# Kernel tuning notes

Hardware: AMD Instinct MI355X
Metric: run time of the kernel (lower is better)

## Reference

```python
import jax, jax.numpy as jnp
import numpy as np
import math

EMBED_DIM = 1024
NUM_HEADS = 16
HEAD_DIM = EMBED_DIM // NUM_HEADS
BLOCK_SIZE = 64
NUM_RAND_BLOCKS = 3
B, L = 2, 2048


def _build_sparse_mask(seq_len, block_size, num_rand_blocks, seed=0):
    """BigBird block-sparse mask: global (first/last block) + window (prev/self/next) + random blocks."""
    nb = seq_len // block_size
    bm = np.zeros((nb, nb), dtype=bool)
    # global: first and last blocks attend to all / are attended by all
    bm[0, :] = True
    bm[:, 0] = True
    bm[-1, :] = True
    bm[:, -1] = True
    # sliding window for interior blocks
    for b in range(1, nb - 1):
        bm[b, max(b - 1, 0):b + 2] = True
    # random blocks for interior blocks (deterministic for reproducibility)
    rng = np.random.default_rng(seed)
    for b in range(1, nb - 1):
        avail = [x for x in range(nb) if x != b]
        picks = rng.permutation(len(avail))[:num_rand_blocks]
        for p in picks:
            bm[b, avail[p]] = True
    # expand block mask to token-level [L, L]
    return np.kron(bm, np.ones((block_size, block_size), dtype=bool))


def setup_inputs() -> dict:
    key = jax.random.key(0)
    k0, k1, k2, k3, k4 = jax.random.split(key, 5)
    hidden_states = jax.random.normal(k0, (B, L, EMBED_DIM), dtype=jnp.float32)
    s = 0.02
    # torch nn.Linear weights have shape [out_features, in_features]
    Wq = jax.random.normal(k1, (EMBED_DIM, EMBED_DIM), dtype=jnp.float32) * s
    Wk = jax.random.normal(k2, (EMBED_DIM, EMBED_DIM), dtype=jnp.float32) * s
    Wv = jax.random.normal(k3, (EMBED_DIM, EMBED_DIM), dtype=jnp.float32) * s
    Wo = jax.random.normal(k4, (EMBED_DIM, EMBED_DIM), dtype=jnp.float32) * s
    sparse_mask = jnp.asarray(_build_sparse_mask(L, BLOCK_SIZE, NUM_RAND_BLOCKS))
    return {"hidden_states": hidden_states, "Wq": Wq, "Wk": Wk, "Wv": Wv,
            "Wo": Wo, "sparse_mask": sparse_mask}


def reference(hidden_states, Wq, Wk, Wv, Wo, sparse_mask):
    Bsz, Lq, D = hidden_states.shape
    H, hd = NUM_HEADS, HEAD_DIM
    # projections (Linear no bias): x @ W.T
    q = (hidden_states @ Wq.T).reshape(Bsz, Lq, H, hd).transpose(0, 2, 1, 3)
    k = (hidden_states @ Wk.T).reshape(Bsz, Lq, H, hd).transpose(0, 2, 1, 3)
    v = (hidden_states @ Wv.T).reshape(Bsz, Lq, H, hd).transpose(0, 2, 1, 3)
    # dense scores with block-sparse mask (matches reference module's math)
    scores = jnp.einsum('bhqd,bhkd->bhqk', q, k) / math.sqrt(hd)  # [B,H,L,L]
    scores = jnp.where(sparse_mask[None, None, :, :], scores, -jnp.inf)
    attn = jax.nn.softmax(scores.astype(jnp.float32), axis=-1).astype(scores.dtype)
    out = jnp.einsum('bhqk,bhkd->bhqd', attn, v)
    out = out.transpose(0, 2, 1, 3).reshape(Bsz, Lq, D)
    out = out @ Wo.T
    return out
```

## Files before the change

kernel.cpp:

```cpp
#include <hip/hip_runtime.h>
#include <hip/hip_bf16.h>
#include <stdint.h>

#define LSEQ   2048
#define DMODEL 1024
#define NHEADS 16
#define HDIM   64
#define NB     32
#define BATCH  2
#define NGRP   38
#define NWG_ATTN (32 * NGRP)

typedef unsigned short u16;
typedef __attribute__((ext_vector_type(8))) __bf16 bf16x8;
typedef __attribute__((ext_vector_type(4))) float f32x4;
typedef __attribute__((ext_vector_type(4))) unsigned int u32x4;
typedef __attribute__((ext_vector_type(4))) u16 u16x4;


__device__ __forceinline__ u16 f2b(float f) {
  unsigned b = __float_as_uint(f);
  return (u16)((b + 0x7FFFu + ((b >> 16) & 1u)) >> 16);
}

__device__ __forceinline__ void lds_dma16(const u16* g, u16* l) {
  __builtin_amdgcn_global_load_lds(
      (__attribute__((address_space(1))) const void*)g,
      (__attribute__((address_space(3))) void*)l, 16, 0, 0);
}

__device__ __forceinline__ bool probe_is_bf16(const void* src) {
  const u16* p = (const u16*)src;
  int cnt = 0;
  #pragma unroll
  for (int i = 0; i < 64; ++i) {
    int e = (p[i] >> 7) & 0xFF;
    cnt += (e >= 100 && e <= 140) ? 1 : 0;
  }
  return cnt >= 48;
}

__device__ __forceinline__ bool mask_block(const void* m, int qb, int kb) {
  const unsigned char* p = (const unsigned char*)m;
  size_t e = (size_t)(qb * 64) * LSEQ + (size_t)kb * 64;
  unsigned char b0 = p[0], b1 = p[1], b2 = p[2];
  if (b0 == 1 && b1 == 1) return p[e] != 0;
  if (b0 == 1 && b1 == 0 && b2 == 1) return ((const u16*)m)[e] != 0;
  if (b0 == 1) return ((const unsigned int*)m)[e] != 0;
  if (b0 == 0x80 && b1 == 0x3f) return ((const u16*)m)[e] != 0;
  return ((const float*)m)[e] != 0.0f;
}

__global__ __launch_bounds__(256) void convert_kernel(
    const void* __restrict__ hs, const void* __restrict__ wq,
    const void* __restrict__ wk, const void* __restrict__ wv,
    const void* __restrict__ wo, u16* __restrict__ dst,
    const void* __restrict__ mask, int* __restrict__ skb,
    f32x4* __restrict__ zbuf, int zn4) {
  __shared__ int sflags;
  if (threadIdx.x == 0)
    sflags = (probe_is_bf16(hs) ? 1 : 0) | (probe_is_bf16(wq) ? 2 : 0);
  __syncthreads();
  bool bf_hs = (sflags & 1) != 0, bf_w = (sflags & 2) != 0;
  if (blockIdx.x == 0 && threadIdx.x < NB) {
    int qb = threadIdx.x;
    int base = (qb == 0) ? 0 : ((qb == 31) ? 32 : (64 + (qb - 1) * 8));
    int cap = (qb == 0 || qb == 31) ? 32 : 8;
    int c = 0;
    for (int kb = 0; kb < NB; ++kb)
      if (mask_block(mask, qb, kb)) skb[base + c++] = kb;
    for (; c < cap; ++c) skb[base + c] = -1;
  }
  const int HS4 = BATCH * LSEQ * DMODEL / 4;
  const int W4 = DMODEL * DMODEL / 4;
  int total4 = HS4 + 4 * W4;
  int stride = gridDim.x * blockDim.x;
  if (!(bf_hs && bf_w)) {
    for (int i = blockIdx.x * blockDim.x + threadIdx.x; i < total4; i += stride) {
      const void* src;
      int off;
      bool isbf;
      if (i < HS4) { src = hs; off = i; isbf = bf_hs; }
      else {
        int j = i - HS4;
        int wsel = j >> 18;
        off = j & (W4 - 1);
        src = (wsel == 0) ? wq : (wsel == 1) ? wk : (wsel == 2) ? wv : wo;
        isbf = bf_w;
      }
      if (isbf) continue;
      f32x4 f = ((const f32x4*)src)[off];
      ((u16x4*)dst)[i] = (u16x4){f2b(f[0]), f2b(f[1]), f2b(f[2]), f2b(f[3])};
    }
  }
  for (int i = blockIdx.x * blockDim.x + threadIdx.x; i < zn4; i += stride)
    zbuf[i] = (f32x4){0.f, 0.f, 0.f, 0.f};
}

#define QBM 256
#define QBN 192

#define BAR()  __builtin_amdgcn_s_barrier()
#define LGK0() asm volatile("s_waitcnt lgkmcnt(0)" ::: "memory")
#define VM3()  asm volatile("s_waitcnt vmcnt(3)" ::: "memory")
#define VM0()  asm volatile("s_waitcnt vmcnt(0)" ::: "memory")

#define STG_A1(p, gi, kt) \
    lds_dma16(Abase + (gi)*65536 + (kt)*64, sA + (p)*16384 + (gi)*4096 + wb8)
#define STG_B1(p, Bgp, kt) \
    lds_dma16((Bgp) + (kt)*64, sB + (p)*12288 + (Bgp##_gi)*4096 + wb8)

#define LDA(afX, p, mh) do { \
    const u16* _ba = sA + (p)*16384 + (wr*128 + (mh)*64 + lc)*64; \
    afX[0][0] = *(const bf16x8*)(_ba +        x0); afX[0][1] = *(const bf16x8*)(_ba +        x1); \
    afX[1][0] = *(const bf16x8*)(_ba + 1024 + x0); afX[1][1] = *(const bf16x8*)(_ba + 1024 + x1); \
    afX[2][0] = *(const bf16x8*)(_ba + 2048 + x0); afX[2][1] = *(const bf16x8*)(_ba + 2048 + x1); \
    afX[3][0] = *(const bf16x8*)(_ba + 3072 + x0); afX[3][1] = *(const bf16x8*)(_ba + 3072 + x1); \
  } while (0)
#define LDB1(p, nh) do { \
    const u16* _bb = sB + (p)*12288 + (wc*48 + (nh)*16 + lc)*64; \
    bfr[nh][0] = *(const bf16x8*)(_bb + x0); bfr[nh][1] = *(const bf16x8*)(_bb + x1); \
  } while (0)

#define MM8(afX, mh, nh) do { \
    __builtin_amdgcn_s_setprio(1); \
    _Pragma("unroll") \
    for (int _m = 0; _m < 4; ++_m) { \
      f32x4 _c = acc[(mh)*4+_m][nh]; \
      _c = __builtin_amdgcn_mfma_f32_16x16x32_bf16(afX[_m][0], bfr[nh][0], _c, 0, 0, 0); \
      _c = __builtin_amdgcn_mfma_f32_16x16x32_bf16(afX[_m][1], bfr[nh][1], _c, 0, 0, 0); \
      acc[(mh)*4+_m][nh] = _c; \
    } \
    __builtin_amdgcn_s_setprio(0); \
  } while (0)

__global__ __launch_bounds__(512, 2) void gemm_qkv(
    const void* __restrict__ hs_raw, const u16* __restrict__ hs_cv,
    const void* __restrict__ wq_r, const void* __restrict__ wk_r,
    const void* __restrict__ wv_r, const u16* __restrict__ wqb_cv,
    u16* __restrict__ C, u16* __restrict__ C2) {
  extern __shared__ u16 smem[];
  u16* sA = smem;
  u16* sB = smem + 2 * 16384;

  const int t = threadIdx.x;
  const int l = t & 63;
  const int w = t >> 6;
  const int wr = w >> 2;
  const int wc = w & 3;
  const int q4 = l >> 4, lc = l & 15;
  const int tileM = blockIdx.x * QBM;
  const int tileN = blockIdx.y * QBN;
  const int sr = t >> 3;
  const int scs = (((t & 7) ^ ((t >> 3) & 7)) * 8);
  const int wb8 = w * 512;
  const int x0 = (q4 ^ (lc & 7)) * 8;
  const int x1 = x0 ^ 32;

  const bool a_bf = probe_is_bf16(hs_raw);
  const bool b_bf = probe_is_bf16(wq_r);
  const u16* Asrc = a_bf ? (const u16*)hs_raw : hs_cv;
  const u16* Abase = Asrc + (size_t)(tileM + sr) * 1024 + scs;
  const u16* Bg0; const u16* Bg1; const u16* Bg2;
  {
    int g0 = tileN, g1 = tileN + 64, g2 = tileN + 128;
    const void* w0 = (g0 >> 10) == 0 ? wq_r : (g0 >> 10) == 1 ? wk_r : wv_r;
    const void* w1 = (g1 >> 10) == 0 ? wq_r : (g1 >> 10) == 1 ? wk_r : wv_r;
    const void* w2 = (g2 >> 10) == 0 ? wq_r : (g2 >> 10) == 1 ? wk_r : wv_r;
    Bg0 = (b_bf ? (const u16*)w0 + (size_t)(g0 & 1023) * 1024
                : wqb_cv + (size_t)g0 * 1024) + (size_t)sr * 1024 + scs;
    Bg1 = (b_bf ? (const u16*)w1 + (size_t)(g1 & 1023) * 1024
                : wqb_cv + (size_t)g1 * 1024) + (size_t)sr * 1024 + scs;
    Bg2 = (b_bf ? (const u16*)w2 + (size_t)(g2 & 1023) * 1024
                : wqb_cv + (size_t)g2 * 1024) + (size_t)sr * 1024 + scs;
  }
  const int Bg0_gi = 0, Bg1_gi = 1, Bg2_gi = 2;

  f32x4 acc[8][3] = {};
  bf16x8 afA[4][2];
  bf16x8 afB[4][2];
  bf16x8 bfr[3][2];

  STG_B1(0, Bg0, 0); STG_B1(0, Bg1, 0); STG_B1(0, Bg2, 0);
  STG_A1(0, 0, 0); STG_A1(0, 1, 0); STG_A1(0, 2, 0); STG_A1(0, 3, 0);
  STG_B1(1, Bg0, 1); STG_B1(1, Bg1, 1); STG_B1(1, Bg2, 1);
  VM3(); BAR();

  #pragma unroll 1
  for (int j = 0; j < 7; ++j) {
    const int kt1 = 2 * j + 1, ktn0 = 2 * j + 2, ktn1 = 2 * j + 3;
    LDA(afA, 0, 0); LDB1(0, 0); LDB1(0, 1); STG_A1(1, 0, kt1); STG_A1(1, 1, kt1);
    BAR(); LGK0(); MM8(afA, 0, 0); MM8(afA, 0, 1); BAR();
    LDB1(0, 2); LDA(afB, 0, 1); STG_A1(1, 2, kt1); STG_A1(1, 3, kt1);
    BAR(); LGK0(); MM8(afA, 0, 2); MM8(afB, 1, 0); BAR();
    STG_B1(0, Bg0, ktn0); STG_B1(0, Bg1, ktn0); STG_B1(0, Bg2, ktn0);
    VM3(); BAR(); MM8(afB, 1, 1); MM8(afB, 1, 2); BAR();
    LDA(afA, 1, 0); LDB1(1, 0); LDB1(1, 1); STG_A1(0, 0, ktn0); STG_A1(0, 1, ktn0);
    BAR(); LGK0(); MM8(afA, 0, 0); MM8(afA, 0, 1); BAR();
    LDB1(1, 2); LDA(afB, 1, 1); STG_A1(0, 2, ktn0); STG_A1(0, 3, ktn0);
    BAR(); LGK0(); MM8(afA, 0, 2); MM8(afB, 1, 0); BAR();
    STG_B1(1, Bg0, ktn1); STG_B1(1, Bg1, ktn1); STG_B1(1, Bg2, ktn1);
    VM3(); BAR(); MM8(afB, 1, 1); MM8(afB, 1, 2); BAR();
  }

  LDA(afA, 0, 0); LDB1(0, 0); LDB1(0, 1); STG_A1(1, 0, 15); STG_A1(1, 1, 15);
  BAR(); LGK0(); MM8(afA, 0, 0); MM8(afA, 0, 1); BAR();
  LDB1(0, 2); LDA(afB, 0, 1); STG_A1(1, 2, 15); STG_A1(1, 3, 15);
  BAR(); LGK0(); MM8(afA, 0, 2); MM8(afB, 1, 0); BAR();
  VM0(); BAR(); MM8(afB, 1, 1); MM8(afB, 1, 2); BAR();
  LDA(afA, 1, 0); LDB1(1, 0); LDB1(1, 1);
  LGK0(); MM8(afA, 0, 0); MM8(afA, 0, 1);
  LDB1(1, 2); LDA(afB, 1, 1);
  LGK0(); MM8(afA, 0, 2); MM8(afB, 1, 0);
  MM8(afB, 1, 1); MM8(afB, 1, 2);

  #pragma unroll
  for (int im = 0; im < 8; ++im)
    #pragma unroll
    for (int jn = 0; jn < 3; ++jn) {
      int rowb = tileM + wr * 128 + im * 16 + q4 * 4;
      int col = tileN + wc * 48 + jn * 16 + lc;
      int sel = col >> 10;
      int o = col & 1023;
      int h = o >> 6, d = o & 63;
      int b = rowb >> 11, ll = rowb & 2047;
      if (sel == 2) {
        u16x4 pk = {f2b(acc[im][jn][0]), f2b(acc[im][jn][1]),
                    f2b(acc[im][jn][2]), f2b(acc[im][jn][3])};
        *(u16x4*)(C2 + ((size_t)((b * NHEADS + h) * HDIM + d)) * LSEQ + ll) = pk;
      } else {
        float scl = (sel == 0) ? 0.125f : 1.0f;
        #pragma unroll
        for (int r = 0; r < 4; ++r) {
          size_t idx = (size_t)sel * (size_t)(BATCH * NHEADS * LSEQ * HDIM) +
                       (((size_t)(b * NHEADS + h) * LSEQ) + ll + r) * HDIM + d;
          C[idx] = f2b(acc[im][jn][r] * scl);
        }
      }
    }
}

#define OTK 32

__global__ __launch_bounds__(256) void gemm_out(
    const u16* __restrict__ A, const void* __restrict__ wo_raw,
    const u16* __restrict__ wo_cv, void* __restrict__ C,
    const void* __restrict__ probe_src) {
  __shared__ u16 lA[128 * OTK];
  __shared__ u16 lB[64 * OTK];
  int t = threadIdx.x;
  int w = t >> 6, l = t & 63, q4 = l >> 4, lc = l & 15;
  int lr = l >> 2, lcc = l & 3;
  int tileM = blockIdx.x * 128, tileN = blockIdx.y * 64;
  int wm = (w >> 1) * 64, wn = (w & 1) * 32;
  bool out_bf = probe_is_bf16(probe_src);
  const u16* Bsrc = probe_is_bf16(wo_raw) ? (const u16*)wo_raw : wo_cv;

  f32x4 acc[4][2] = {};

  for (int kt = 0; kt < 1024; kt += OTK) {
    __syncthreads();
    #pragma unroll
    for (int it = 0; it < 2; ++it) {
      int m = w * 2 + it;
      int row = m * 16 + lr;
      lds_dma16(A + (size_t)(tileM + row) * 1024 + kt + lcc * 8, lA + m * 512);
    }
    {
      int row = w * 16 + lr;
      lds_dma16(Bsrc + (size_t)(tileN + row) * 1024 + kt + lcc * 8, lB + w * 512);
    }
    __syncthreads();
    bf16x8 af[4], bf[2];
    #pragma unroll
    for (int i = 0; i < 4; ++i)
      af[i] = *(const bf16x8*)(lA + (wm + i * 16 + lc) * OTK + q4 * 8);
    #pragma unroll
    for (int j = 0; j < 2; ++j)
      bf[j] = *(const bf16x8*)(lB + (wn + j * 16 + lc) * OTK + q4 * 8);
    #pragma unroll
    for (int i = 0; i < 4; ++i)
      #pragma unroll
      for (int j = 0; j < 2; ++j)
        acc[i][j] = __builtin_amdgcn_mfma_f32_16x16x32_bf16(af[i], bf[j], acc[i][j], 0, 0, 0);
  }

  #pragma unroll
  for (int i = 0; i < 4; ++i)
    #pragma unroll
    for (int j = 0; j < 2; ++j) {
      int rowb = tileM + wm + i * 16 + q4 * 4;
      int col = tileN + wn + j * 16 + lc;
      #pragma unroll
      for (int r = 0; r < 4; ++r) {
        float v = acc[i][j][r];
        size_t idx = (size_t)(rowb + r) * 1024 + col;
        if (out_bf) ((u16*)C)[idx] = f2b(v);
        else ((float*)C)[idx] = v;
      }
    }
}

#define LDP 72

__global__ __launch_bounds__(256) void attn_kernel(
    const u16* __restrict__ qb_, const u16* __restrict__ kb_,
    const u16* __restrict__ vt_, const int* __restrict__ skb,
    float* __restrict__ obuf2, float* __restrict__ lbuf2,
    u16* __restrict__ ctx) {
  __shared__ u16 lK[2][64 * 64];
  __shared__ u16 lV[2][64 * 64];
  __shared__ u16 lP[4][16 * LDP];
  int i = blockIdx.x;
  int bh = (i & 7) + ((i >> 3) & 3) * 8;
  int g = i >> 5;
  int qb = (g < 4) ? 0 : ((g < 8) ? 31 : (g - 7));
  int t = threadIdx.x, w = t >> 6, l = t & 63, q4 = l >> 4, lc = l & 15;
  int r0 = t >> 3, r1 = 32 + (t >> 3);
  int scc = ((t & 7) ^ ((t >> 3) & 7)) * 8;
  const int x0 = (q4 ^ (lc & 7)) * 8;
  const int x1 = x0 ^ 32;

  const u16* qp = qb_ + ((size_t)bh * LSEQ + qb * 64 + w * 16 + lc) * HDIM;
  bf16x8 bq0 = *(const bf16x8*)(qp + q4 * 8);
  bf16x8 bq1 = *(const bf16x8*)(qp + 32 + q4 * 8);

  const u16* kp = kb_ + (size_t)bh * LSEQ * HDIM;
  const u16* vp = vt_ + (size_t)bh * HDIM * LSEQ;
  u16* myP = &lP[w][0];

  f32x4 oacc[4];
  #pragma unroll
  for (int d = 0; d < 4; ++d) oacc[d] = (f32x4){0.f, 0.f, 0.f, 0.f};
  float lp = 0.0f;

  int nkb = 0;
  #pragma unroll
  for (int j = 0; j < 8; ++j) nkb += (skb[g * 8 + j] >= 0) ? 1 : 0;

  auto STAGE = [&](int it, int buf) {
    int kb = skb[g * 8 + it];
    const u16* kblk = kp + (size_t)kb * 64 * HDIM;
    const u16* vblk = vp + kb * 64;
    u16* dK = &lK[buf][0];
    u16* dV = &lV[buf][0];
    lds_dma16(kblk + r0 * HDIM + scc, dK + w * 512);
    lds_dma16(kblk + r1 * HDIM + scc, dK + 2048 + w * 512);
    lds_dma16(vblk + (size_t)r0 * LSEQ + scc, dV + w * 512);
    lds_dma16(vblk + (size_t)r1 * LSEQ + scc, dV + 2048 + w * 512);
  };

  STAGE(0, 0);
  __syncthreads();

  for (int it = 0; it < nkb; ++it) {
    int buf = it & 1;
    if (it + 1 < nkb) STAGE(it + 1, buf ^ 1);
    const u16* bK = &lK[buf][0];
    const u16* bV = &lV[buf][0];

    f32x4 st[4];
    #pragma unroll
    for (int mt = 0; mt < 4; ++mt) {
      const u16* kr = bK + (mt * 16 + lc) * 64;
      bf16x8 k0 = *(const bf16x8*)(kr + x0);
      bf16x8 k1 = *(const bf16x8*)(kr + x1);
      f32x4 z = (f32x4){0.f, 0.f, 0.f, 0.f};
      z = __builtin_amdgcn_mfma_f32_16x16x32_bf16(k0, bq0, z, 0, 0, 0);
      z = __builtin_amdgcn_mfma_f32_16x16x32_bf16(k1, bq1, z, 0, 0, 0);
      st[mt] = z;
    }

    #pragma unroll
    for (int mt = 0; mt < 4; ++mt) {
      float p0 = __expf(st[mt][0]), p1 = __expf(st[mt][1]);
      float p2 = __expf(st[mt][2]), p3 = __expf(st[mt][3]);
      lp += (p0 + p1) + (p2 + p3);
      u16x4 pk = {f2b(p0), f2b(p1), f2b(p2), f2b(p3)};
      *(u16x4*)(myP + lc * LDP + mt * 16 + q4 * 4) = pk;
    }

    bf16x8 ap0 = *(const bf16x8*)(myP + lc * LDP + q4 * 8);
    bf16x8 ap1 = *(const bf16x8*)(myP + lc * LDP + 32 + q4 * 8);
    #pragma unroll
    for (int dt = 0; dt < 4; ++dt) {
      const u16* vr = bV + (dt * 16 + lc) * 64;
      bf16x8 v0 = *(const bf16x8*)(vr + x0);
      bf16x8 v1 = *(const bf16x8*)(vr + x1);
      oacc[dt] = __builtin_amdgcn_mfma_f32_16x16x32_bf16(ap0, v0, oacc[dt], 0, 0, 0);
      oacc[dt] = __builtin_amdgcn_mfma_f32_16x16x32_bf16(ap1, v1, oacc[dt], 0, 0, 0);
    }

    __syncthreads();
  }

  float ltot = lp;
  ltot += __shfl_xor(ltot, 16);
  ltot += __shfl_xor(ltot, 32);

  if (g >= 8) {
    float inv[4];
    #pragma unroll
    for (int r = 0; r < 4; ++r)
      inv[r] = 1.0f / __shfl(ltot, q4 * 4 + r);
    int b = bh >> 4, h = bh & 15;
    #pragma unroll
    for (int dt = 0; dt < 4; ++dt)
      #pragma unroll
      for (int r = 0; r < 4; ++r) {
        float v = oacc[dt][r] * inv[r];
        int grow = qb * 64 + w * 16 + q4 * 4 + r;
        size_t odx = ((size_t)b * LSEQ + grow) * DMODEL + h * HDIM + dt * 16 + lc;
        ctx[odx] = f2b(v);
      }
  } else {
    int s = (qb == 31) ? 1 : 0;
    if (q4 == 0)
      unsafeAtomicAdd(lbuf2 + ((size_t)bh * 2 + s) * 64 + w * 16 + lc, ltot);
    #pragma unroll
    for (int dt = 0; dt < 4; ++dt)
      #pragma unroll
      for (int r = 0; r < 4; ++r)
        unsafeAtomicAdd(obuf2 + (((size_t)bh * 2 + s) * 64 + w * 16 + q4 * 4 + r) * 64 +
                            dt * 16 + lc, oacc[dt][r]);
  }
}

__global__ __launch_bounds__(256) void normalize2_kernel(
    const float* __restrict__ obuf2, const float* __restrict__ lbuf2,
    u16* __restrict__ ctx) {
  int e4 = blockIdx.x * 256 + threadIdx.x;
  int e = e4 * 4;
  int bh = e >> 13;
  int rem = e & 8191;
  int s = rem >> 12, row = (rem >> 6) & 63, d = rem & 63;
  f32x4 o = *(const f32x4*)(obuf2 + e);
  float linv = 1.0f / lbuf2[(bh * 2 + s) * 64 + row];
  int qb = s ? 31 : 0;
  int b = bh >> 4, h = bh & 15;
  int grow = qb * 64 + row;
  u16x4 pk = {f2b(o[0] * linv), f2b(o[1] * linv), f2b(o[2] * linv), f2b(o[3] * linv)};
  *(u16x4*)(ctx + ((size_t)b * LSEQ + grow) * DMODEL + h * HDIM + d) = pk;
}

extern "C" void kernel_launch(void* const* d_in, const int* in_sizes, int n_in,
                              void* d_out, int out_size, void* d_ws, size_t ws_size,
                              hipStream_t stream) {
  const void* hs = d_in[0];
  const void* wq = d_in[1];
  const void* wk = d_in[2];
  const void* wv = d_in[3];
  const void* wo = d_in[4];
  const void* mask = d_in[5];

  u16* hsb = (u16*)d_ws;
  u16* wqb = hsb + 4 * 1024 * 1024;
  u16* wob = wqb + 3 * 1024 * 1024;
  u16* qbuf = wob + 1024 * 1024;
  u16* kbuf = qbuf + 4 * 1024 * 1024;
  u16* vtb  = kbuf + 4 * 1024 * 1024;
  u16* ctx  = vtb + 4 * 1024 * 1024;
  int* skb  = (int*)(ctx + 4 * 1024 * 1024);
  float* obuf2 = (float*)(skb + 512);
  float* lbuf2 = obuf2 + 32 * 2 * 64 * 64;
  const int ZN4 = (32 * 2 * 64 * 64 + 4096) / 4;

  static bool attr_done = false;
  if (!attr_done) {
    hipFuncSetAttribute((const void*)gemm_qkv,
                        hipFuncAttributeMaxDynamicSharedMemorySize, 114688);
    attr_done = true;
  }

  convert_kernel<<<4096, 256, 0, stream>>>(hs, wq, wk, wv, wo, hsb, mask, skb,
                                           (f32x4*)obuf2, ZN4);

  dim3 gqkv(16, 16);
  gemm_qkv<<<gqkv, 512, 114688, stream>>>(hs, hsb, wq, wk, wv, wqb, qbuf, vtb);

  attn_kernel<<<NWG_ATTN, 256, 0, stream>>>(qbuf, kbuf, vtb, skb, obuf2, lbuf2, ctx);

  normalize2_kernel<<<256, 256, 0, stream>>>(obuf2, lbuf2, ctx);

  dim3 gout(32, 16);
  gemm_out<<<gout, 256, 0, stream>>>(ctx, wo, wob, d_out, hs);
}
```

Measured before the change: 192.3 us.

## Widen output GEMM tile, use exp2 softmax, replace global-row atomics with partial buffers

The output projection GEMM tile grows from 128x64 to 128x128, giving each wave 4x4 MFMA accumulators and halving the grid so each A tile is reused across more columns. The Q scale now folds in log2(e), so the attention kernel can use exp2f in place of __expf. The global-query-block workgroups no longer do float atomics into a shared accumulator. Each writes its own partial slice, and the normalize kernel sums the four partials. This removes atomic contention but uses more workspace, enlarges the zero-init region, and raises register pressure in gemm_out.

```diff
diff --git a/kernel.cpp b/kernel.cpp
--- a/kernel.cpp
+++ b/kernel.cpp
@@ -1,6 +1,7 @@
 #include <hip/hip_runtime.h>
 #include <hip/hip_bf16.h>
 #include <stdint.h>
+#include <math.h>
 
 #define LSEQ   2048
 #define DMODEL 1024
@@ -229,7 +230,7 @@
                     f2b(acc[im][jn][2]), f2b(acc[im][jn][3])};
         *(u16x4*)(C2 + ((size_t)((b * NHEADS + h) * HDIM + d)) * LSEQ + ll) = pk;
       } else {
-        float scl = (sel == 0) ? 0.125f : 1.0f;
+        float scl = (sel == 0) ? 0.18033688f : 1.0f;
         #pragma unroll
         for (int r = 0; r < 4; ++r) {
           size_t idx = (size_t)sel * (size_t)(BATCH * NHEADS * LSEQ * HDIM) +
@@ -247,16 +248,16 @@
     const u16* __restrict__ wo_cv, void* __restrict__ C,
     const void* __restrict__ probe_src) {
   __shared__ u16 lA[128 * OTK];
-  __shared__ u16 lB[64 * OTK];
+  __shared__ u16 lB[128 * OTK];
   int t = threadIdx.x;
   int w = t >> 6, l = t & 63, q4 = l >> 4, lc = l & 15;
   int lr = l >> 2, lcc = l & 3;
-  int tileM = blockIdx.x * 128, tileN = blockIdx.y * 64;
-  int wm = (w >> 1) * 64, wn = (w & 1) * 32;
+  int tileM = blockIdx.x * 128, tileN = blockIdx.y * 128;
+  int wm = (w >> 1) * 64, wn = (w & 1) * 64;
   bool out_bf = probe_is_bf16(probe_src);
   const u16* Bsrc = probe_is_bf16(wo_raw) ? (const u16*)wo_raw : wo_cv;
 
-  f32x4 acc[4][2] = {};
+  f32x4 acc[4][4] = {};
 
   for (int kt = 0; kt < 1024; kt += OTK) {
     __syncthreads();
@@ -265,30 +266,27 @@
       int m = w * 2 + it;
       int row = m * 16 + lr;
       lds_dma16(A + (size_t)(tileM + row) * 1024 + kt + lcc * 8, lA + m * 512);
-    }
-    {
-      int row = w * 16 + lr;
-      lds_dma16(Bsrc + (size_t)(tileN + row) * 1024 + kt + lcc * 8, lB + w * 512);
+      lds_dma16(Bsrc + (size_t)(tileN + row) * 1024 + kt + lcc * 8, lB + m * 512);
     }
     __syncthreads();
-    bf16x8 af[4], bf[2];
+    bf16x8 af[4], bf[4];
     #pragma unroll
     for (int i = 0; i < 4; ++i)
       af[i] = *(const bf16x8*)(lA + (wm + i * 16 + lc) * OTK + q4 * 8);
     #pragma unroll
-    for (int j = 0; j < 2; ++j)
+    for (int j = 0; j < 4; ++j)
       bf[j] = *(const bf16x8*)(lB + (wn + j * 16 + lc) * OTK + q4 * 8);
     #pragma unroll
     for (int i = 0; i < 4; ++i)
       #pragma unroll
-      for (int j = 0; j < 2; ++j)
+      for (int j = 0; j < 4; ++j)
         acc[i][j] = __builtin_amdgcn_mfma_f32_16x16x32_bf16(af[i], bf[j], acc[i][j], 0, 0, 0);
   }
 
   #pragma unroll
   for (int i = 0; i < 4; ++i)
     #pragma unroll
-    for (int j = 0; j < 2; ++j) {
+    for (int j = 0; j < 4; ++j) {
       int rowb = tileM + wm + i * 16 + q4 * 4;
       int col = tileN + wn + j * 16 + lc;
       #pragma unroll
@@ -373,8 +371,8 @@
 
     #pragma unroll
     for (int mt = 0; mt < 4; ++mt) {
-      float p0 = __expf(st[mt][0]), p1 = __expf(st[mt][1]);
-      float p2 = __expf(st[mt][2]), p3 = __expf(st[mt][3]);
+      float p0 = exp2f(st[mt][0]), p1 = exp2f(st[mt][1]);
+      float p2 = exp2f(st[mt][2]), p3 = exp2f(st[mt][3]);
       lp += (p0 + p1) + (p2 + p3);
       u16x4 pk = {f2b(p0), f2b(p1), f2b(p2), f2b(p3)};
       *(u16x4*)(myP + lc * LDP + mt * 16 + q4 * 4) = pk;
@@ -415,14 +413,15 @@
       }
   } else {
     int s = (qb == 31) ? 1 : 0;
+    int wgi = g & 3;
+    float* ob = obuf2 + ((size_t)((bh * 2 + s) * 4 + wgi)) * 4096;
     if (q4 == 0)
-      unsafeAtomicAdd(lbuf2 + ((size_t)bh * 2 + s) * 64 + w * 16 + lc, ltot);
+      lbuf2[((bh * 2 + s) * 4 + wgi) * 64 + w * 16 + lc] = ltot;
     #pragma unroll
     for (int dt = 0; dt < 4; ++dt)
       #pragma unroll
       for (int r = 0; r < 4; ++r)
-        unsafeAtomicAdd(obuf2 + (((size_t)bh * 2 + s) * 64 + w * 16 + q4 * 4 + r) * 64 +
-                            dt * 16 + lc, oacc[dt][r]);
+        ob[(w * 16 + q4 * 4 + r) * 64 + dt * 16 + lc] = oacc[dt][r];
   }
 }
 
@@ -434,8 +433,14 @@
   int bh = e >> 13;
   int rem = e & 8191;
   int s = rem >> 12, row = (rem >> 6) & 63, d = rem & 63;
-  f32x4 o = *(const f32x4*)(obuf2 + e);
-  float linv = 1.0f / lbuf2[(bh * 2 + s) * 64 + row];
+  const float* base = obuf2 + ((size_t)(bh * 2 + s) * 4) * 4096 + row * 64 + d;
+  f32x4 o = *(const f32x4*)(base);
+  o += *(const f32x4*)(base + 4096);
+  o += *(const f32x4*)(base + 8192);
+  o += *(const f32x4*)(base + 12288);
+  int lb = (bh * 2 + s) * 4 * 64 + row;
+  float lsum = lbuf2[lb] + lbuf2[lb + 64] + lbuf2[lb + 128] + lbuf2[lb + 192];
+  float linv = 1.0f / lsum;
   int qb = s ? 31 : 0;
   int b = bh >> 4, h = bh & 15;
   int grow = qb * 64 + row;
@@ -462,13 +467,13 @@
   u16* ctx  = vtb + 4 * 1024 * 1024;
   int* skb  = (int*)(ctx + 4 * 1024 * 1024);
   float* obuf2 = (float*)(skb + 512);
-  float* lbuf2 = obuf2 + 32 * 2 * 64 * 64;
-  const int ZN4 = (32 * 2 * 64 * 64 + 4096) / 4;
+  float* lbuf2 = obuf2 + 32 * 2 * 4 * 64 * 64;
+  const int ZN4 = (32 * 2 * 4 * 64 * 64 + 16384) / 4;
 
   static bool attr_done = false;
   if (!attr_done) {
-    hipFuncSetAttribute((const void*)gemm_qkv,
-                        hipFuncAttributeMaxDynamicSharedMemorySize, 114688);
+    (void)hipFuncSetAttribute((const void*)gemm_qkv,
+                              hipFuncAttributeMaxDynamicSharedMemorySize, 114688);
     attr_done = true;
   }
 
@@ -482,6 +487,6 @@
 
   normalize2_kernel<<<256, 256, 0, stream>>>(obuf2, lbuf2, ctx);
 
-  dim3 gout(32, 16);
+  dim3 gout(32, 8);
   gemm_out<<<gout, 256, 0, stream>>>(ctx, wo, wob, d_out, hs);
 }
```

Result: slower. 202.8 us (+5.5%).
